# Performance work log

Hardware: AMD Instinct MI355X
Metric: run time of the kernel (lower is better)

The kernel has to match this reference:

```python
import jax, jax.numpy as jnp
import numpy as np

B, S, D, H, HD, I, L = 1, 2048, 1024, 16, 64, 2816, 2
EPS = 1e-5
ROPE_BASE = 10000.0


def rmsnorm(x, w):
    return x * jax.lax.rsqrt(jnp.mean(x * x, axis=-1, keepdims=True) + EPS) * w


def precompute_freqs_cis():
    # matches precompute_freqs_cis: [S, HD//2, 2] = (cos, sin)
    freqs = 1.0 / (ROPE_BASE ** (jnp.arange(0, HD, 2, dtype=jnp.float32) / HD))
    ang = jnp.outer(jnp.arange(S, dtype=jnp.float32), freqs)
    return jnp.stack([jnp.cos(ang), jnp.sin(ang)], axis=-1)


def apply_rope(x, fc):
    # x: [B,S,H,HD]; fc: [S,HD//2,2] -> interleaved pair rotation
    xs = x.reshape(*x.shape[:-1], HD // 2, 2)
    f = fc[None, :, None]  # [1,S,1,HD//2,2]
    out = jnp.stack([
        xs[..., 0] * f[..., 0] - xs[..., 1] * f[..., 1],
        xs[..., 1] * f[..., 0] + xs[..., 0] * f[..., 1],
    ], axis=-1)
    return out.reshape(x.shape)


def setup_inputs() -> dict:
    key = jax.random.key(0)
    ks = jax.random.split(key, 6)
    p = lambda k, shape: jax.random.normal(k, shape, jnp.float32) * 0.02
    return {
        "x": jax.random.normal(ks[0], (B, S, D), jnp.float32),
        "wqkv": p(ks[1], (L, 3 * H * HD, D)),
        "wo": p(ks[2], (L, D, H * HD)),
        "w1": p(ks[3], (L, I, D)),
        "w2": p(ks[4], (L, D, I)),
        "w3": p(ks[5], (L, I, D)),
        "attn_norm_w": jnp.ones((L, D), jnp.float32),
        "ffn_norm_w": jnp.ones((L, D), jnp.float32),
        "attn_ls": 0.01 * jnp.ones((L, D), jnp.float32),
        "ffn_ls": 0.01 * jnp.ones((L, D), jnp.float32),
        "final_norm_w": jnp.ones((D,), jnp.float32),
    }


def reference(x, wqkv, wo, w1, w2, w3, attn_norm_w, ffn_norm_w, attn_ls, ffn_ls, final_norm_w):
    fc = precompute_freqs_cis()
    causal = jnp.tril(jnp.ones((S, S), dtype=bool))  # [S,S]
    scale = 1.0 / np.sqrt(HD).astype(np.float32)
    h = x
    for l in range(L):
        # --- attention block ---
        xn = rmsnorm(h, attn_norm_w[l])
        qkv = xn @ wqkv[l].T  # [B,S,3*H*HD]
        q, k, v = jnp.split(qkv, 3, axis=-1)
        q = apply_rope(q.reshape(B, S, H, HD), fc)
        k = apply_rope(k.reshape(B, S, H, HD), fc)
        v = v.reshape(B, S, H, HD)
        scores = jnp.einsum('bqhd,bkhd->bhqk', q, k) * scale
        scores = jnp.where(causal, scores, jnp.finfo(scores.dtype).min)
        attn = jax.nn.softmax(scores, axis=-1)
        y = jnp.einsum('bhqk,bkhd->bqhd', attn, v).reshape(B, S, H * HD)
        h = h + (y @ wo[l].T) * attn_ls[l]
        # --- feed-forward block (SwiGLU) ---
        xn = rmsnorm(h, ffn_norm_w[l])
        ff = (jax.nn.silu(xn @ w1[l].T) * (xn @ w3[l].T)) @ w2[l].T
        h = h + ff * ffn_ls[l]
    return rmsnorm(h, final_norm_w)
```

## Files before the change

kernel.cpp:

```cpp
#include <hip/hip_runtime.h>
#include <math.h>

#define SEQ 2048
#define DIM 1024
#define NH 16
#define HDIM 64
#define IDIM 2816
#define NL 2

typedef __attribute__((ext_vector_type(8))) short bf16x8;
typedef __attribute__((ext_vector_type(4))) float f32x4;

__device__ __forceinline__ unsigned short f2bf(float f) {
    unsigned int u = __float_as_uint(f);
    u = (u + 0x7fffu + ((u >> 16) & 1u)) >> 16;
    return (unsigned short)u;
}
__device__ __forceinline__ float bf2f(unsigned short u) {
    return __uint_as_float((unsigned int)u << 16);
}

__device__ __forceinline__ void gl_lds16(const void* g, void* l) {
    __builtin_amdgcn_global_load_lds(
        (const __attribute__((address_space(1))) unsigned int*)g,
        (__attribute__((address_space(3))) unsigned int*)l, 16, 0, 0);
}

#define WAITVM(n) asm volatile("s_waitcnt vmcnt(" #n ")" ::: "memory")
#define BARRIER_PIN()                       \
    do {                                    \
        __builtin_amdgcn_s_barrier();       \
        __builtin_amdgcn_sched_barrier(0);  \
    } while (0)

template <bool BF16OUT>
__global__ __launch_bounds__(256) void rmsnorm_kernel(const float* __restrict__ in,
                                                      const float* __restrict__ w,
                                                      void* __restrict__ out) {
    const int row = blockIdx.x;
    const int t = threadIdx.x;
    const float4 v = ((const float4*)(in + (size_t)row * DIM))[t];
    float ss = v.x * v.x + v.y * v.y + v.z * v.z + v.w * v.w;
#pragma unroll
    for (int m = 1; m < 64; m <<= 1) ss += __shfl_xor(ss, m);
    __shared__ float red[4];
    if ((t & 63) == 0) red[t >> 6] = ss;
    __syncthreads();
    const float tot = red[0] + red[1] + red[2] + red[3];
    const float r = 1.0f / sqrtf(tot * (1.0f / DIM) + 1e-5f);
    const float4 wv = ((const float4*)w)[t];
    float o0 = v.x * r * wv.x, o1 = v.y * r * wv.y;
    float o2 = v.z * r * wv.z, o3 = v.w * r * wv.w;
    if (BF16OUT) {
        ushort4 o = {f2bf(o0), f2bf(o1), f2bf(o2), f2bf(o3)};
        ((ushort4*)((unsigned short*)out + (size_t)row * DIM))[t] = o;
    } else {
        float4 o = {o0, o1, o2, o3};
        ((float4*)((float*)out + (size_t)row * DIM))[t] = o;
    }
}

#define WQKV_OFF 0
#define WO_OFF   3145728
#define W1_OFF   4194304
#define W3_OFF   7077888
#define W2_OFF   9961472
#define WTOT     12845056

__global__ __launch_bounds__(256) void convert_weights_kernel(
    const float* __restrict__ wqkv, const float* __restrict__ wo,
    const float* __restrict__ w1, const float* __restrict__ w3,
    const float* __restrict__ w2, unsigned short* __restrict__ out) {
    const size_t i8 = ((size_t)blockIdx.x * 256 + threadIdx.x) * 8;
    const float* src;
    size_t local;
    if (i8 < WO_OFF)      { src = wqkv; local = i8 - WQKV_OFF; }
    else if (i8 < W1_OFF) { src = wo;   local = i8 - WO_OFF; }
    else if (i8 < W3_OFF) { src = w1;   local = i8 - W1_OFF; }
    else if (i8 < W2_OFF) { src = w3;   local = i8 - W3_OFF; }
    else                  { src = w2;   local = i8 - W2_OFF; }
    const float4 v0 = *(const float4*)(src + local);
    const float4 v1 = *(const float4*)(src + local + 4);
    ushort4 o0 = {f2bf(v0.x), f2bf(v0.y), f2bf(v0.z), f2bf(v0.w)};
    ushort4 o1 = {f2bf(v1.x), f2bf(v1.y), f2bf(v1.z), f2bf(v1.w)};
    *(ushort4*)(out + i8) = o0;
    *(ushort4*)(out + i8 + 4) = o1;
}

template <int EPI, int BM, int BN, int KSPLIT>
__global__ __launch_bounds__(256) void mfma_gemm(
    const unsigned short* __restrict__ A,
    const unsigned short* __restrict__ B,
    const unsigned short* __restrict__ Bhi, int nsplit,
    float* __restrict__ Cf,
    unsigned short* __restrict__ Cb,
    const float* __restrict__ ls,
    int N, int K) {
    constexpr int MI = BM / 32;
    constexpr int NJ = BN / 32;
    constexpr int L = (BM + BN) / 32;
    static_assert(L == 6 || L == 8, "WAITVM literals cover L=6,8");
    __shared__ unsigned short As[2][BM * 64];
    __shared__ unsigned short Bs[2][BN * 64];

    const int tid = threadIdx.x;

    const int nwg = gridDim.x * gridDim.y;
    const int orig = blockIdx.y * gridDim.x + blockIdx.x;
    const int swz = (orig & 7) * (nwg >> 3) + (orig >> 3);
    const int bx = swz / gridDim.y;
    const int by = swz % gridDim.y;
    const int m0 = by * BM;
    const int ncol0 = bx * BN;

    const unsigned short* Bp = B;
    int n0 = ncol0;
    if (n0 >= nsplit) { Bp = Bhi; n0 -= nsplit; }

    const int Koff = (KSPLIT > 1) ? blockIdx.z * (K / KSPLIT) : 0;

    const int r0 = tid >> 3;
    const int cswz = (tid & 7) ^ (r0 & 7);
    const unsigned short* Ag = A + (size_t)(m0 + r0) * K + Koff + cswz * 8;
    const unsigned short* Bg = Bp + (size_t)(n0 + r0) * K + Koff + cswz * 8;

    const int lane = tid & 63;
    const int wid = tid >> 6;
    const int wr = (wid >> 1) * (BM / 2);
    const int wc = (wid & 1) * (BN / 2);
    const int fr = lane & 15;
    const int hi = lane >> 4;

    f32x4 acc[MI][NJ] = {};

    auto stage = [&](int buf, int kk) {
#pragma unroll
        for (int q = 0; q < BM / 32; ++q)
            gl_lds16(Ag + (size_t)(q * 32) * K + kk, &As[buf][q * 2048 + tid * 8]);
#pragma unroll
        for (int q = 0; q < BN / 32; ++q)
            gl_lds16(Bg + (size_t)(q * 32) * K + kk, &Bs[buf][q * 2048 + tid * 8]);
    };

    auto frag = [&](const unsigned short* base, int R, int c) -> bf16x8 {
        return *(const bf16x8*)&base[R * 64 + ((c ^ (R & 7)) << 3)];
    };

    auto compute_tile = [&](int buf) {
        bf16x8 a[MI][2], b[NJ][2];
#pragma unroll
        for (int m = 0; m < MI; ++m)
#pragma unroll
            for (int kw = 0; kw < 2; ++kw)
                a[m][kw] = frag(As[buf], wr + m * 16 + fr, kw * 4 + hi);
#pragma unroll
        for (int n = 0; n < NJ; ++n)
#pragma unroll
            for (int kw = 0; kw < 2; ++kw)
                b[n][kw] = frag(Bs[buf], wc + n * 16 + fr, kw * 4 + hi);
        __builtin_amdgcn_s_setprio(1);
#pragma unroll
        for (int kw = 0; kw < 2; ++kw)
#pragma unroll
            for (int m = 0; m < MI; ++m)
#pragma unroll
                for (int n = 0; n < NJ; ++n)
                    acc[m][n] = __builtin_amdgcn_mfma_f32_16x16x32_bf16(
                        a[m][kw], b[n][kw], acc[m][n], 0, 0, 0);
        __builtin_amdgcn_s_setprio(0);
    };

    const int NT = K / KSPLIT / 64;

    stage(0, 0);
    stage(1, 64);

    int buf = 0;
    for (int t = 0; t < NT - 1; ++t) {
        if constexpr (L == 6) WAITVM(6); else WAITVM(8);
        BARRIER_PIN();
        compute_tile(buf);
        asm volatile("s_waitcnt lgkmcnt(0)" ::: "memory");
        BARRIER_PIN();
        if (t + 2 < NT) stage(buf, (t + 2) * 64);
        buf ^= 1;
    }
    WAITVM(0);
    BARRIER_PIN();
    compute_tile(buf);

    const int erow = m0 + wr + hi * 4;
    const int ecol = ncol0 + wc + fr;
#pragma unroll
    for (int m = 0; m < MI; ++m) {
#pragma unroll
        for (int n = 0; n < NJ; ++n) {
            const f32x4 v = acc[m][n];
            const int row = erow + m * 16;
            const int col = ecol + n * 16;
            if (EPI == 1) {
                const float lv = ls[col];
#pragma unroll
                for (int j = 0; j < 4; ++j) {
                    float* p = Cf + (size_t)(row + j) * N + col;
                    if (KSPLIT > 1) atomicAdd(p, v[j] * lv);
                    else            *p = *p + v[j] * lv;
                }
            } else {
#pragma unroll
                for (int j = 0; j < 4; ++j)
                    Cb[(size_t)(row + j) * N + col] = f2bf(v[j]);
            }
        }
    }
}

__global__ __launch_bounds__(256) void silu_mul_kernel(
    const unsigned short* __restrict__ c13,
    unsigned short* __restrict__ outp) {
    const size_t e8 = ((size_t)blockIdx.x * 256 + threadIdx.x) * 8;
    const int m = (int)(e8 / IDIM);
    const int i = (int)(e8 % IDIM);
    const unsigned short* g = c13 + (size_t)m * (2 * IDIM) + i;
    const bf16x8 gv = *(const bf16x8*)g;
    const bf16x8 uv = *(const bf16x8*)(g + IDIM);
    unsigned short o[8];
#pragma unroll
    for (int j = 0; j < 8; ++j) {
        const float x = bf2f((unsigned short)gv[j]);
        const float u = bf2f((unsigned short)uv[j]);
        o[j] = f2bf(x / (1.0f + __expf(-x)) * u);
    }
    *(bf16x8*)(outp + (size_t)m * IDIM + i) = *(const bf16x8*)o;
}

__global__ __launch_bounds__(256) void rope_split_kernel(
    const unsigned short* __restrict__ qkv,
    unsigned short* __restrict__ Qh,
    unsigned short* __restrict__ Kh,
    unsigned short* __restrict__ Vt) {
    const int st = blockIdx.x;
    const int h = blockIdx.y;
    const int tid = threadIdx.x;
    const int srow = tid >> 2;
    const int scol = (tid & 3) * 16;
    const int s = st * 64 + srow;
    __shared__ unsigned short Vl[64][72];

    const unsigned short* base = qkv + (size_t)s * (3 * DIM) + h * HDIM + scol;

    unsigned short qv[16], kv[16], vv[16];
    *(bf16x8*)&qv[0] = *(const bf16x8*)(base);
    *(bf16x8*)&qv[8] = *(const bf16x8*)(base + 8);
    *(bf16x8*)&kv[0] = *(const bf16x8*)(base + DIM);
    *(bf16x8*)&kv[8] = *(const bf16x8*)(base + DIM + 8);
    *(bf16x8*)&vv[0] = *(const bf16x8*)(base + 2 * DIM);
    *(bf16x8*)&vv[8] = *(const bf16x8*)(base + 2 * DIM + 8);

    const float FC = -0.28782313662425572f;
    unsigned short qo[16], ko[16];
#pragma unroll
    for (int i = 0; i < 8; ++i) {
        const int p = scol / 2 + i;
        const float freq = __expf(FC * (float)p);
        const float ang = (float)s * freq;
        float sn, cs;
        sincosf(ang, &sn, &cs);
        const float q0 = bf2f(qv[2 * i]), q1 = bf2f(qv[2 * i + 1]);
        const float k0 = bf2f(kv[2 * i]), k1 = bf2f(kv[2 * i + 1]);
        qo[2 * i]     = f2bf(q0 * cs - q1 * sn);
        qo[2 * i + 1] = f2bf(q1 * cs + q0 * sn);
        ko[2 * i]     = f2bf(k0 * cs - k1 * sn);
        ko[2 * i + 1] = f2bf(k1 * cs + k0 * sn);
    }
    unsigned short* qdst = Qh + ((size_t)h * SEQ + s) * HDIM + scol;
    unsigned short* kdst = Kh + ((size_t)h * SEQ + s) * HDIM + scol;
    *(bf16x8*)qdst = *(const bf16x8*)&qo[0];
    *(bf16x8*)(qdst + 8) = *(const bf16x8*)&qo[8];
    *(bf16x8*)kdst = *(const bf16x8*)&ko[0];
    *(bf16x8*)(kdst + 8) = *(const bf16x8*)&ko[8];

#pragma unroll
    for (int i = 0; i < 16; ++i) Vl[scol + i][srow] = vv[i];
    __syncthreads();
    const int d = tid >> 2;
    const int c0 = (tid & 3) * 16;
    unsigned short* vdst = Vt + ((size_t)h * HDIM + d) * SEQ + st * 64 + c0;
    *(bf16x8*)vdst = *(const bf16x8*)&Vl[d][c0];
    *(bf16x8*)(vdst + 8) = *(const bf16x8*)&Vl[d][c0 + 8];
}

__global__ __launch_bounds__(256) void attn_mfma_kernel(
    const unsigned short* __restrict__ Qh,
    const unsigned short* __restrict__ Kh,
    const unsigned short* __restrict__ Vt,
    unsigned short* __restrict__ y) {
    const int h = blockIdx.x;
    const int qt = blockIdx.y;
    const int qb = (qt < 16) ? qt : 47 - qt;

    __shared__ unsigned short Ql[64][72];
    __shared__ unsigned short Kl[2][64][72];
    __shared__ unsigned short Vl[2][64][72];
    __shared__ unsigned short Pl[64][72];

    const int tid = threadIdx.x;
    const int lane = tid & 63;
    const int w = tid >> 6;
    const int fr = lane & 15;
    const int fk = (lane >> 4) * 8;
    const int rg = (lane >> 4) * 4;
    const int srow = tid >> 2;
    const int sc8 = (tid & 3) * 8;

    {
        const unsigned short* src = Qh + ((size_t)h * SEQ + qb * 64 + srow) * HDIM + sc8;
        *(bf16x8*)&Ql[srow][sc8] = *(const bf16x8*)src;
        *(bf16x8*)&Ql[srow][sc8 + 32] = *(const bf16x8*)(src + 32);
    }
    __syncthreads();
    bf16x8 qa[2];
    qa[0] = *(const bf16x8*)&Ql[w * 16 + fr][fk];
    qa[1] = *(const bf16x8*)&Ql[w * 16 + fr][32 + fk];

    bf16x8 kr0, kr1, vr0, vr1;
    {
        const unsigned short* ks = Kh + ((size_t)h * SEQ + srow) * HDIM + sc8;
        kr0 = *(const bf16x8*)ks;
        kr1 = *(const bf16x8*)(ks + 32);
        const unsigned short* vs = Vt + ((size_t)h * HDIM + srow) * SEQ + sc8;
        vr0 = *(const bf16x8*)vs;
        vr1 = *(const bf16x8*)(vs + 32);
    }

    float l_[4] = {0.0f, 0.0f, 0.0f, 0.0f};
    f32x4 O[4] = {};

    for (int kb = 0; kb <= qb; ++kb) {
        const int cur = kb & 1;
        *(bf16x8*)&Kl[cur][srow][sc8] = kr0;
        *(bf16x8*)&Kl[cur][srow][sc8 + 32] = kr1;
        *(bf16x8*)&Vl[cur][srow][sc8] = vr0;
        *(bf16x8*)&Vl[cur][srow][sc8 + 32] = vr1;
        __syncthreads();

        if (kb < qb) {
            const unsigned short* ks = Kh + ((size_t)h * SEQ + (kb + 1) * 64 + srow) * HDIM + sc8;
            kr0 = *(const bf16x8*)ks;
            kr1 = *(const bf16x8*)(ks + 32);
            const unsigned short* vs = Vt + ((size_t)h * HDIM + srow) * SEQ + (kb + 1) * 64 + sc8;
            vr0 = *(const bf16x8*)vs;
            vr1 = *(const bf16x8*)(vs + 32);
        }

        f32x4 sa[4] = {};
        __builtin_amdgcn_s_setprio(1);
#pragma unroll
        for (int ks2 = 0; ks2 < 2; ++ks2)
#pragma unroll
            for (int n = 0; n < 4; ++n) {
                const bf16x8 kf = *(const bf16x8*)&Kl[cur][n * 16 + fr][ks2 * 32 + fk];
                sa[n] = __builtin_amdgcn_mfma_f32_16x16x32_bf16(qa[ks2], kf, sa[n], 0, 0, 0);
            }
        __builtin_amdgcn_s_setprio(0);

        const bool diag = (kb == qb);
#pragma unroll
        for (int n = 0; n < 4; ++n) {
            const int col = n * 16 + fr;
#pragma unroll
            for (int j = 0; j < 4; ++j) {
                const float sv = sa[n][j] * 0.125f;
                float e = __expf(fminf(sv, 30.0f));
                if (diag && col > rg + j) e = 0.0f;
                l_[j] += e;
                Pl[w * 16 + rg + j][col] = f2bf(e);
            }
        }

        __builtin_amdgcn_s_setprio(1);
#pragma unroll
        for (int ks2 = 0; ks2 < 2; ++ks2) {
            const bf16x8 pa = *(const bf16x8*)&Pl[w * 16 + fr][ks2 * 32 + fk];
#pragma unroll
            for (int nd = 0; nd < 4; ++nd) {
                const bf16x8 vf = *(const bf16x8*)&Vl[cur][nd * 16 + fr][ks2 * 32 + fk];
                O[nd] = __builtin_amdgcn_mfma_f32_16x16x32_bf16(pa, vf, O[nd], 0, 0, 0);
            }
        }
        __builtin_amdgcn_s_setprio(0);
    }

#pragma unroll
    for (int j = 0; j < 4; ++j) {
#pragma unroll
        for (int msk = 1; msk < 16; msk <<= 1) l_[j] += __shfl_xor(l_[j], msk);
    }

#pragma unroll
    for (int j = 0; j < 4; ++j) {
        const float inv = 1.0f / l_[j];
        unsigned short* dst = y + (size_t)(qb * 64 + w * 16 + rg + j) * DIM + h * HDIM + fr;
#pragma unroll
        for (int nd = 0; nd < 4; ++nd)
            dst[nd * 16] = f2bf(O[nd][j] * inv);
    }
}

extern "C" void kernel_launch(void* const* d_in, const int* in_sizes, int n_in,
                              void* d_out, int out_size, void* d_ws, size_t ws_size,
                              hipStream_t stream) {
    const float* x            = (const float*)d_in[0];
    const float* wqkv         = (const float*)d_in[1];
    const float* wo           = (const float*)d_in[2];
    const float* w1           = (const float*)d_in[3];
    const float* w2           = (const float*)d_in[4];
    const float* w3           = (const float*)d_in[5];
    const float* attn_norm_w  = (const float*)d_in[6];
    const float* ffn_norm_w   = (const float*)d_in[7];
    const float* attn_ls      = (const float*)d_in[8];
    const float* ffn_ls       = (const float*)d_in[9];
    const float* final_norm_w = (const float*)d_in[10];
    float* out = (float*)d_out;

    char* ws = (char*)d_ws;
    float*          h     = (float*)ws;
    unsigned short* xnb   = (unsigned short*)(ws + 8388608);
    unsigned short* yb    = (unsigned short*)(ws + 12582912);
    unsigned short* qkvb  = (unsigned short*)(ws + 16777216);
    unsigned short* Qhb   = (unsigned short*)(ws + 29360128);
    unsigned short* Khb   = (unsigned short*)(ws + 33554432);
    unsigned short* Vtb   = (unsigned short*)(ws + 37748736);
    unsigned short* c13   = (unsigned short*)(ws + 16777216);
    unsigned short* ffb   = (unsigned short*)(ws + 41943040);
    unsigned short* wbuf  = (unsigned short*)(ws + 46137344);

    unsigned short* wqkv_b = wbuf + WQKV_OFF;
    unsigned short* wo_b   = wbuf + WO_OFF;
    unsigned short* w1_b   = wbuf + W1_OFF;
    unsigned short* w3_b   = wbuf + W3_OFF;
    unsigned short* w2_b   = wbuf + W2_OFF;

    const int BIG = 1 << 30;

    hipMemcpyAsync(h, x, (size_t)SEQ * DIM * sizeof(float),
                   hipMemcpyDeviceToDevice, stream);

    for (int l = 0; l < NL; ++l) {
        convert_weights_kernel<<<WTOT / 2048, 256, 0, stream>>>(
            wqkv + (size_t)l * 3 * DIM * DIM, wo + (size_t)l * DIM * DIM,
            w1 + (size_t)l * IDIM * DIM, w3 + (size_t)l * IDIM * DIM,
            w2 + (size_t)l * DIM * IDIM, wbuf);

        rmsnorm_kernel<true><<<SEQ, 256, 0, stream>>>(h, attn_norm_w + l * DIM, xnb);
        mfma_gemm<3, 128, 128, 1><<<dim3(3 * DIM / 128, SEQ / 128), 256, 0, stream>>>(
            xnb, wqkv_b, nullptr, BIG, nullptr, qkvb, nullptr, 3 * DIM, DIM);
        rope_split_kernel<<<dim3(SEQ / 64, NH), 256, 0, stream>>>(qkvb, Qhb, Khb, Vtb);
        attn_mfma_kernel<<<dim3(NH, SEQ / 64), 256, 0, stream>>>(Qhb, Khb, Vtb, yb);
        mfma_gemm<1, 64, 128, 2><<<dim3(DIM / 128, SEQ / 64, 2), 256, 0, stream>>>(
            yb, wo_b, nullptr, BIG, h, nullptr, attn_ls + l * DIM, DIM, DIM);

        rmsnorm_kernel<true><<<SEQ, 256, 0, stream>>>(h, ffn_norm_w + l * DIM, xnb);
        mfma_gemm<3, 128, 128, 1><<<dim3(2 * IDIM / 128, SEQ / 128), 256, 0, stream>>>(
            xnb, w1_b, w3_b, IDIM, nullptr, c13, nullptr, 2 * IDIM, DIM);
        silu_mul_kernel<<<SEQ * IDIM / 2048, 256, 0, stream>>>(c13, ffb);
        mfma_gemm<1, 64, 128, 2><<<dim3(DIM / 128, SEQ / 64, 2), 256, 0, stream>>>(
            ffb, w2_b, nullptr, BIG, h, nullptr, ffn_ls + l * DIM, DIM, IDIM);
    }

    rmsnorm_kernel<false><<<SEQ, 256, 0, stream>>>(h, final_norm_w, out);
}
```

Before: 357.9 us.

## Load A fragments directly from global into registers, staging only B in LDS

The GEMM no longer stages the A tile through shared memory. Each lane loads its MFMA A fragments straight from global memory into double-buffered registers, which two unrolled iterations alternate between. Only B still goes through LDS. This cuts LDS traffic and footprint, and the QKV GEMM switches to a 64-row tile for more workgroups. The cost is uncoalesced, duplicated A reads across the two column-warps and more VGPR use; the vmcnt wait counts were retuned to match.

Measured after the change: 438.5 us. 1.23x slower.

```diff
diff --git a/kernel.cpp b/kernel.cpp
--- a/kernel.cpp
+++ b/kernel.cpp
@@ -98,9 +98,7 @@
     int N, int K) {
     constexpr int MI = BM / 32;
     constexpr int NJ = BN / 32;
-    constexpr int L = (BM + BN) / 32;
-    static_assert(L == 6 || L == 8, "WAITVM literals cover L=6,8");
-    __shared__ unsigned short As[2][BM * 64];
+    static_assert((BM == 64 || BM == 128) && BN == 128, "shape");
     __shared__ unsigned short Bs[2][BN * 64];
 
     const int tid = threadIdx.x;
@@ -121,7 +119,6 @@
 
     const int r0 = tid >> 3;
     const int cswz = (tid & 7) ^ (r0 & 7);
-    const unsigned short* Ag = A + (size_t)(m0 + r0) * K + Koff + cswz * 8;
     const unsigned short* Bg = Bp + (size_t)(n0 + r0) * K + Koff + cswz * 8;
 
     const int lane = tid & 63;
@@ -131,33 +128,35 @@
     const int fr = lane & 15;
     const int hi = lane >> 4;
 
+    const unsigned short* Ag = A + (size_t)(m0 + wr + fr) * K + Koff + hi * 8;
+
     f32x4 acc[MI][NJ] = {};
 
-    auto stage = [&](int buf, int kk) {
-#pragma unroll
-        for (int q = 0; q < BM / 32; ++q)
-            gl_lds16(Ag + (size_t)(q * 32) * K + kk, &As[buf][q * 2048 + tid * 8]);
+    auto stageB = [&](int buf, int kk) {
 #pragma unroll
         for (int q = 0; q < BN / 32; ++q)
             gl_lds16(Bg + (size_t)(q * 32) * K + kk, &Bs[buf][q * 2048 + tid * 8]);
     };
 
-    auto frag = [&](const unsigned short* base, int R, int c) -> bf16x8 {
+    auto loadA = [&](bf16x8 (&ar)[MI][2], int tt) {
+#pragma unroll
+        for (int m = 0; m < MI; ++m)
+#pragma unroll
+            for (int kw = 0; kw < 2; ++kw)
+                ar[m][kw] = *(const bf16x8*)(Ag + (size_t)(m * 16) * K + tt * 64 + kw * 32);
+    };
+
+    auto bfrag = [&](const unsigned short* base, int R, int c) -> bf16x8 {
         return *(const bf16x8*)&base[R * 64 + ((c ^ (R & 7)) << 3)];
     };
 
-    auto compute_tile = [&](int buf) {
-        bf16x8 a[MI][2], b[NJ][2];
-#pragma unroll
-        for (int m = 0; m < MI; ++m)
+    auto compute_tile = [&](int buf, const bf16x8 (&ar)[MI][2]) {
+        bf16x8 b[NJ][2];
+#pragma unroll
+        for (int n = 0; n < NJ; ++n)
 #pragma unroll
             for (int kw = 0; kw < 2; ++kw)
-                a[m][kw] = frag(As[buf], wr + m * 16 + fr, kw * 4 + hi);
-#pragma unroll
-        for (int n = 0; n < NJ; ++n)
-#pragma unroll
-            for (int kw = 0; kw < 2; ++kw)
-                b[n][kw] = frag(Bs[buf], wc + n * 16 + fr, kw * 4 + hi);
+                b[n][kw] = bfrag(Bs[buf], wc + n * 16 + fr, kw * 4 + hi);
         __builtin_amdgcn_s_setprio(1);
 #pragma unroll
         for (int kw = 0; kw < 2; ++kw)
@@ -166,28 +165,46 @@
 #pragma unroll
                 for (int n = 0; n < NJ; ++n)
                     acc[m][n] = __builtin_amdgcn_mfma_f32_16x16x32_bf16(
-                        a[m][kw], b[n][kw], acc[m][n], 0, 0, 0);
+                        ar[m][kw], b[n][kw], acc[m][n], 0, 0, 0);
         __builtin_amdgcn_s_setprio(0);
     };
 
+#define WAIT_STEADY()                                      \
+    do {                                                   \
+        if constexpr (MI == 4) { WAITVM(12); }             \
+        else                   { WAITVM(8); }              \
+    } while (0)
+
+#define GEMM_ITER(AR, TT, DO_STAGE, LAST)                  \
+    {                                                      \
+        if (LAST) { WAITVM(0); } else { WAIT_STEADY(); }   \
+        BARRIER_PIN();                                     \
+        compute_tile((TT) & 1, AR);                        \
+        asm volatile("s_waitcnt lgkmcnt(0)" ::: "memory"); \
+        BARRIER_PIN();                                     \
+        if (DO_STAGE) {                                    \
+            stageB((TT) & 1, ((TT) + 2) * 64);             \
+            loadA(AR, (TT) + 2);                           \
+        }                                                  \
+    }
+
     const int NT = K / KSPLIT / 64;
 
-    stage(0, 0);
-    stage(1, 64);
-
-    int buf = 0;
-    for (int t = 0; t < NT - 1; ++t) {
-        if constexpr (L == 6) WAITVM(6); else WAITVM(8);
-        BARRIER_PIN();
-        compute_tile(buf);
-        asm volatile("s_waitcnt lgkmcnt(0)" ::: "memory");
-        BARRIER_PIN();
-        if (t + 2 < NT) stage(buf, (t + 2) * 64);
-        buf ^= 1;
-    }
-    WAITVM(0);
-    BARRIER_PIN();
-    compute_tile(buf);
+    bf16x8 aR0[MI][2], aR1[MI][2];
+    stageB(0, 0);
+    loadA(aR0, 0);
+    stageB(1, 64);
+    loadA(aR1, 1);
+
+    for (int t = 0; t < NT - 2; t += 2) {
+        GEMM_ITER(aR0, t, true, false);
+        GEMM_ITER(aR1, t + 1, (t + 3) < NT, false);
+    }
+    GEMM_ITER(aR0, NT - 2, false, false);
+    GEMM_ITER(aR1, NT - 1, false, true);
+
+#undef GEMM_ITER
+#undef WAIT_STEADY
 
     const int erow = m0 + wr + hi * 4;
     const int ecol = ncol0 + wc + fr;
@@ -453,7 +470,7 @@
             w2 + (size_t)l * DIM * IDIM, wbuf);
 
         rmsnorm_kernel<true><<<SEQ, 256, 0, stream>>>(h, attn_norm_w + l * DIM, xnb);
-        mfma_gemm<3, 128, 128, 1><<<dim3(3 * DIM / 128, SEQ / 128), 256, 0, stream>>>(
+        mfma_gemm<3, 64, 128, 1><<<dim3(3 * DIM / 128, SEQ / 64), 256, 0, stream>>>(
             xnb, wqkv_b, nullptr, BIG, nullptr, qkvb, nullptr, 3 * DIM, DIM);
         rope_split_kernel<<<dim3(SEQ / 64, NH), 256, 0, stream>>>(qkvb, Qhb, Khb, Vtb);
         attn_mfma_kernel<<<dim3(NH, SEQ / 64), 256, 0, stream>>>(Qhb, Khb, Vtb, yb);
```
